# Kernel optimization log

Measured on AMD Instinct MI355X. Metric: run time of the kernel, lower is better.

The kernel has to match this reference:

```python
import jax, jax.numpy as jnp
import numpy as np
import math

B, S, E, H = 4, 1024, 1024, 16
D = E // H
C = 1.0           # Poincare ball curvature
CS = math.sqrt(C)
EPS = 1e-7

def _sq(x):
    return jnp.sum(x * x, axis=-1, keepdims=True)

def expmap0(v):
    n = jnp.sqrt(jnp.clip(_sq(v), 1e-15))
    return jnp.tanh(CS * n) * v / (CS * n)

def logmap0(y):
    n = jnp.sqrt(jnp.clip(_sq(y), 1e-15))
    t = jnp.clip(CS * n, 0.0, 1.0 - 1e-6)
    return jnp.arctanh(t) * y / (CS * n)

def hlinear(x, z, r):
    # Poincare fully-connected layer (HNN++, Shimizu et al.), as in hypll HLinear
    lam = 2.0 / jnp.clip(1.0 - C * _sq(x), EPS)          # [..., 1] conformal factor
    zn = jnp.clip(jnp.linalg.norm(z, axis=0), 1e-15)     # [out]
    xz = x @ z                                           # [..., out]
    tcr = 2.0 * CS * r
    v = (2.0 * zn / CS) * jnp.arcsinh(CS * lam * xz / zn * jnp.cosh(tcr) - (lam - 1.0) * jnp.sinh(tcr))
    w = jnp.sinh(CS * v) / CS
    return w / (1.0 + jnp.sqrt(1.0 + C * jnp.sum(w * w, -1, keepdims=True)))

def _beta(a, b):
    return math.exp(math.lgamma(a) + math.lgamma(b) - math.lgamma(a + b))

def _forward(query, key, value, zq, bq, zk, bk, zv, bv):
    pq, pk, pv = hlinear(query, zq, bq), hlinear(key, zk, bk), hlinear(value, zv, bv)
    split = lambda x: x.reshape(B, S, H, D).transpose(0, 2, 1, 3)   # [B,H,S,D]
    q, k, v = split(pq), split(pk), split(pv)
    # attention_similarity: negative per-head pairwise Poincare distance (all heads vectorized)
    q2 = jnp.sum(q * q, -1)                              # [B,H,Sq]
    k2 = jnp.sum(k * k, -1)                              # [B,H,Sk]
    qk = jnp.einsum('bhqd,bhkd->bhqk', q, k)
    diff2 = jnp.clip(q2[..., :, None] + k2[..., None, :] - 2.0 * qk, 0.0)
    den = jnp.clip((1.0 - C * q2)[..., :, None] * (1.0 - C * k2)[..., None, :], EPS)
    dist = jnp.arccosh(jnp.clip(1.0 + 2.0 * C * diff2 / den, 1.0 + 1e-6)) / CS
    # attention_activation: softmax over keys
    w = jax.nn.softmax(-dist, axis=-1)                   # [B,H,Sq,Sk]
    # attention_midpoint: weighted gyromidpoint of values over keys
    lam = 2.0 / jnp.clip(1.0 - C * jnp.sum(v * v, -1), EPS)          # [B,H,Sk]
    num = jnp.einsum('bhqk,bhkd->bhqd', w * lam[..., None, :], v)
    dnm = jnp.clip(jnp.einsum('bhqk,bhk->bhq', jnp.abs(w), lam - 1.0), EPS)
    u = num / dnm[..., None]
    mid = u / (1.0 + jnp.sqrt(jnp.clip(1.0 - C * _sq(u), EPS)))      # (1/2) Mobius scalar mult
    # manifold.cat: beta-concatenation of heads (HNN++)
    scale = _beta(E / 2.0, 0.5) / _beta(D / 2.0, 0.5)
    tv = logmap0(mid) * scale                            # tangent at origin, [B,H,S,D]
    return expmap0(tv.transpose(0, 2, 1, 3).reshape(B, S, E))

def setup_inputs():
    key = jax.random.key(0)
    ks = jax.random.split(key, 9)
    mk = lambda k: expmap0(jax.random.normal(k, (B, S, E), jnp.float32) * (0.3 / math.sqrt(E)))
    zs = lambda k: jax.random.normal(k, (E, E), jnp.float32) / math.sqrt(E)
    bs = lambda k: jax.random.normal(k, (E,), jnp.float32) * 0.01
    return {"query": mk(ks[0]), "key": mk(ks[1]), "value": mk(ks[2]),
            "zq": zs(ks[3]), "bq": bs(ks[4]), "zk": zs(ks[5]), "bk": bs(ks[6]),
            "zv": zs(ks[7]), "bv": bs(ks[8])}

def reference(query, key, value, zq, bq, zk, bk, zv, bv):
    return _forward(query, key, value, zq, bq, zk, bk, zv, bv)
```

## Files before the change

kernel.cpp:

```cpp
#include <hip/hip_runtime.h>
#include <cmath>

#define EPSF 1e-7f

constexpr int B_ = 4, S_ = 1024, E_ = 1024, H_ = 16, D_ = 64;
constexpr int BS_ = B_ * S_;

typedef __attribute__((ext_vector_type(8))) short bf16x8;
typedef __attribute__((ext_vector_type(4))) float f32x4;

__device__ inline unsigned int fbits(float f) { union { float f; unsigned int u; } x; x.f = f; return x.u; }
__device__ inline float ubits(unsigned int u) { union { unsigned int u; float f; } x; x.u = u; return x.f; }

__device__ inline unsigned short f2bf(float f) {
  unsigned int u = fbits(f);
  unsigned int r = u + 0x7fffu + ((u >> 16) & 1u);
  return (unsigned short)(r >> 16);
}
__device__ inline float bf2f(unsigned short h) { return ubits(((unsigned int)h) << 16); }
__device__ inline float fastrcp(float x) { return __builtin_amdgcn_rcpf(x); }

__device__ inline unsigned int packhi(float a, float b) {
  return (fbits(a) >> 16) | (fbits(b) & 0xFFFF0000u);
}
__device__ inline unsigned int packlo(float a, float b) {
  float la = a - ubits(fbits(a) & 0xFFFF0000u);
  float lb = b - ubits(fbits(b) & 0xFFFF0000u);
  return (fbits(la) >> 16) | (fbits(lb) & 0xFFFF0000u);
}

__device__ __forceinline__ void async_ld16(const unsigned short* g, unsigned short* l) {
  __builtin_amdgcn_global_load_lds(
      (const __attribute__((address_space(1))) unsigned int*)g,
      (__attribute__((address_space(3))) unsigned int*)l, 16, 0, 0);
}

__global__ __launch_bounds__(256) void xsplit_kernel(
    const float* __restrict__ xq, const float* __restrict__ xk,
    const float* __restrict__ xv, unsigned short* __restrict__ Xbf,
    float* __restrict__ lamRow) {
  const int row = blockIdx.x;
  const float* x = (row < BS_) ? xq : (row < 2 * BS_ ? xk : xv);
  const int r = row & (BS_ - 1);
  const int tid = threadIdx.x;
  float4 v = ((const float4*)(x + (size_t)r * E_))[tid];
  float s = v.x * v.x + v.y * v.y + v.z * v.z + v.w * v.w;
  #pragma unroll
  for (int m = 1; m < 64; m <<= 1) s += __shfl_xor(s, m, 64);
  __shared__ float red[4];
  if ((tid & 63) == 0) red[tid >> 6] = s;
  __syncthreads();
  s = red[0] + red[1] + red[2] + red[3];
  uint2 p;
  p.x = (unsigned int)f2bf(v.x) | ((unsigned int)f2bf(v.y) << 16);
  p.y = (unsigned int)f2bf(v.z) | ((unsigned int)f2bf(v.w) << 16);
  ((uint2*)(Xbf + (size_t)row * E_))[tid] = p;
  if (tid == 0) lamRow[row] = 2.0f / fmaxf(1.0f - s, EPSF);
}

__global__ __launch_bounds__(256) void zsplit_kernel(
    const float* __restrict__ zq, const float* __restrict__ zk, const float* __restrict__ zv,
    unsigned short* __restrict__ BhiT, unsigned short* __restrict__ BloT,
    float* __restrict__ Zpart) {
  const int mat = blockIdx.z;
  const float* z = mat == 0 ? zq : (mat == 1 ? zk : zv);
  const int k0 = blockIdx.y * 64, n0 = blockIdx.x * 64;
  __shared__ float t[64][65];
  __shared__ float sred[64][4];
  const int tid = threadIdx.x;
  {
    int kr = tid >> 4, nc = (tid & 15) * 4;
    #pragma unroll
    for (int i = 0; i < 4; i++) {
      float4 vv = *(const float4*)(z + (size_t)(k0 + kr + i * 16) * E_ + n0 + nc);
      t[kr + i * 16][nc + 0] = vv.x;
      t[kr + i * 16][nc + 1] = vv.y;
      t[kr + i * 16][nc + 2] = vv.z;
      t[kr + i * 16][nc + 3] = vv.w;
    }
  }
  __syncthreads();
  int nr = tid >> 2, kc = (tid & 3) * 16;
  unsigned int ph[8], pl[8];
  float ss = 0.f;
  #pragma unroll
  for (int p = 0; p < 8; p++) {
    float x0 = t[kc + 2 * p][nr], x1 = t[kc + 2 * p + 1][nr];
    ph[p] = packhi(x0, x1);
    pl[p] = packlo(x0, x1);
    ss += x0 * x0 + x1 * x1;
  }
  size_t off = (size_t)mat * E_ * E_ + (size_t)(n0 + nr) * E_ + k0 + kc;
  uint4* dh = (uint4*)(BhiT + off);
  uint4* dl = (uint4*)(BloT + off);
  dh[0] = make_uint4(ph[0], ph[1], ph[2], ph[3]);
  dh[1] = make_uint4(ph[4], ph[5], ph[6], ph[7]);
  dl[0] = make_uint4(pl[0], pl[1], pl[2], pl[3]);
  dl[1] = make_uint4(pl[4], pl[5], pl[6], pl[7]);
  sred[nr][tid & 3] = ss;
  __syncthreads();
  if (tid < 64) {
    float v = sred[tid][0] + sred[tid][1] + sred[tid][2] + sred[tid][3];
    Zpart[(size_t)(mat * 16 + blockIdx.y) * E_ + n0 + tid] = v;
  }
}

__global__ __launch_bounds__(256) void zstat_final_kernel(
    const float* __restrict__ Zpart,
    const float* __restrict__ bq, const float* __restrict__ bk, const float* __restrict__ bv,
    float* __restrict__ znA, float* __restrict__ chA, float* __restrict__ shA) {
  const int idx = blockIdx.x * 256 + threadIdx.x;
  const int mat = idx >> 10, col = idx & 1023;
  const float* bb = mat == 0 ? bq : (mat == 1 ? bk : bv);
  float s = 0.f;
  #pragma unroll
  for (int ky = 0; ky < 16; ky++)
    s += Zpart[(size_t)(mat * 16 + ky) * E_ + col];
  float n = fmaxf(sqrtf(s), 1e-15f);
  znA[idx] = n;
  float rb = bb[col];
  chA[idx] = coshf(2.f * rb);
  shA[idx] = sinhf(2.f * rb);
}

__global__ __launch_bounds__(256, 3) void hlinear_mfma_kernel(
    const unsigned short* __restrict__ Xbf,
    const unsigned short* __restrict__ BhiT, const unsigned short* __restrict__ BloT,
    const float* __restrict__ lamRow, const float* __restrict__ znA,
    const float* __restrict__ chA, const float* __restrict__ shA,
    unsigned short* __restrict__ Wbf) {
  const int mat = blockIdx.z;
  const unsigned short* xa = Xbf + (size_t)mat * BS_ * E_;
  const unsigned short* bh = BhiT + (size_t)mat * E_ * E_;
  const unsigned short* bl = BloT + (size_t)mat * E_ * E_;
  const int lid = blockIdx.y * 8 + blockIdx.x;
  const int sqi = lid >> 4, offb = lid & 15;
  const int m0 = ((sqi >> 1) * 4 + (offb & 3)) * 128;
  const int n0 = ((sqi & 1) * 4 + (offb >> 2)) * 128;

  __shared__ unsigned short LDSU[24576];
  unsigned short* As = LDSU;
  unsigned short* Bh = LDSU + 8192;
  unsigned short* Bl = LDSU + 16384;

  const int tid = threadIdx.x;
  const int wid = tid >> 6, lane = tid & 63, quad = lane >> 4, l16 = lane & 15;
  const int wm = (wid >> 1) * 64, wn = (wid & 1) * 64;

  f32x4 acc[4][4];
  #pragma unroll
  for (int i = 0; i < 4; i++)
    #pragma unroll
    for (int j = 0; j < 4; j++) acc[i][j] = (f32x4){0.f, 0.f, 0.f, 0.f};

  const int lrow = lane >> 3;
  const int lcs = ((lane & 7) ^ lrow) * 8;
  const int xsw = (l16 & 7);

  for (int kt = 0; kt < E_ / 64; ++kt) {
    __syncthreads();
    const int kb = kt * 64 + lcs;
    #pragma unroll
    for (int c2 = 0; c2 < 4; c2++) {
      const int c = wid * 4 + c2;
      const int grow = c * 8 + lrow;
      async_ld16(xa + (size_t)(m0 + grow) * E_ + kb, As + c * 512);
      async_ld16(bh + (size_t)(n0 + grow) * E_ + kb, Bh + c * 512);
      async_ld16(bl + (size_t)(n0 + grow) * E_ + kb, Bl + c * 512);
    }
    __syncthreads();
    #pragma unroll
    for (int h = 0; h < 2; h++) {
      bf16x8 a[4];
      #pragma unroll
      for (int mt = 0; mt < 4; mt++) {
        int row = wm + mt * 16 + l16;
        a[mt] = *(const bf16x8*)&As[row * 64 + (((h * 4 + quad) ^ xsw) * 8)];
      }
      #pragma unroll
      for (int nt = 0; nt < 4; nt++) {
        int row = wn + nt * 16 + l16;
        int ro = row * 64 + (((h * 4 + quad) ^ xsw) * 8);
        bf16x8 bhf = *(const bf16x8*)&Bh[ro];
        bf16x8 blf = *(const bf16x8*)&Bl[ro];
        #pragma unroll
        for (int mt = 0; mt < 4; mt++) {
          acc[mt][nt] = __builtin_amdgcn_mfma_f32_16x16x32_bf16(a[mt], bhf, acc[mt][nt], 0, 0, 0);
          acc[mt][nt] = __builtin_amdgcn_mfma_f32_16x16x32_bf16(a[mt], blf, acc[mt][nt], 0, 0, 0);
        }
      }
    }
  }

  const float* lamP = lamRow + mat * BS_;
  float lamv[16];
  #pragma unroll
  for (int mt = 0; mt < 4; mt++)
    #pragma unroll
    for (int r = 0; r < 4; r++)
      lamv[mt * 4 + r] = lamP[m0 + wm + mt * 16 + quad * 4 + r];

  __syncthreads();
  unsigned short* epi = LDSU + wid * 4608;
  #pragma unroll
  for (int nt = 0; nt < 4; nt++) {
    int cg = n0 + wn + nt * 16 + l16;
    float zn = znA[mat * E_ + cg];
    float chzn = chA[mat * E_ + cg] / zn;
    float sh = shA[mat * E_ + cg];
    float tzn = 2.f * zn;
    #pragma unroll
    for (int mt = 0; mt < 4; mt++) {
      #pragma unroll
      for (int r = 0; r < 4; r++) {
        float lam = lamv[mt * 4 + r];
        float arg = fmaf(lam * acc[mt][nt][r], chzn, -(lam - 1.f) * sh);
        float sq2 = sqrtf(fmaf(arg, arg, 1.f));
        float v = tzn * __logf(arg + sq2);
        float ev = __expf(v);
        float w = 0.5f * (ev - fastrcp(ev));
        epi[(mt * 16 + quad * 4 + r) * 72 + nt * 16 + l16] = f2bf(w);
      }
    }
  }
  unsigned short* gout = Wbf + (size_t)mat * BS_ * E_ + (size_t)(m0 + wm) * E_ + n0 + wn;
  const int rrow = lane >> 3, seg = lane & 7;
  #pragma unroll
  for (int i = 0; i < 8; i++) {
    int row = i * 8 + rrow;
    uint4 val = *(const uint4*)&epi[row * 72 + seg * 8];
    *(uint4*)(gout + (size_t)row * E_ + seg * 8) = val;
  }
}

__global__ __launch_bounds__(256) void normalize_kernel(
    const unsigned short* __restrict__ Wbf, unsigned short* __restrict__ Pbf,
    float* __restrict__ HN) {
  const unsigned short* w = Wbf + (size_t)blockIdx.x * E_;
  int tid = threadIdx.x;
  uint2 wv = ((const uint2*)w)[tid];
  float w0 = bf2f((unsigned short)(wv.x & 0xFFFF));
  float w1 = bf2f((unsigned short)(wv.x >> 16));
  float w2 = bf2f((unsigned short)(wv.y & 0xFFFF));
  float w3 = bf2f((unsigned short)(wv.y >> 16));
  float s = w0 * w0 + w1 * w1 + w2 * w2 + w3 * w3;
  #pragma unroll
  for (int m = 1; m < 64; m <<= 1) s += __shfl_xor(s, m, 64);
  __shared__ float red[4];
  if ((tid & 63) == 0) red[tid >> 6] = s;
  __syncthreads();
  s = red[0] + red[1] + red[2] + red[3];
  float t = 1.f / (1.f + sqrtf(1.f + s));
  unsigned short p0 = f2bf(w0 * t), p1 = f2bf(w1 * t), p2 = f2bf(w2 * t), p3 = f2bf(w3 * t);
  uint2 pk;
  pk.x = (unsigned int)p0 | ((unsigned int)p1 << 16);
  pk.y = (unsigned int)p2 | ((unsigned int)p3 << 16);
  ((uint2*)(Pbf + (size_t)blockIdx.x * E_))[tid] = pk;
  float r0 = bf2f(p0), r1 = bf2f(p1), r2 = bf2f(p2), r3 = bf2f(p3);
  float hs = r0 * r0 + r1 * r1 + r2 * r2 + r3 * r3;
  hs += __shfl_xor(hs, 1, 64);
  hs += __shfl_xor(hs, 2, 64);
  hs += __shfl_xor(hs, 4, 64);
  hs += __shfl_xor(hs, 8, 64);
  if ((tid & 15) == 0) HN[(size_t)blockIdx.x * H_ + (tid >> 4)] = hs;
}

__global__ __launch_bounds__(256) void vtrans_kernel(
    const unsigned short* __restrict__ Pbf, const float* __restrict__ HN,
    unsigned short* __restrict__ VtG, unsigned short* __restrict__ lamMG) {
  const int st = blockIdx.x, h = blockIdx.y, b = blockIdx.z;
  const unsigned short* pv = Pbf + (size_t)2 * BS_ * E_;
  const float* hnv = HN + (size_t)2 * BS_ * H_;
  __shared__ unsigned short T[64][72];
  __shared__ float lamS[64];
  const int tid = threadIdx.x;
  {
    int lr = tid >> 2, lc = (tid & 3) * 16;
    const uint4* src = (const uint4*)(pv + (size_t)(b * S_ + st * 64 + lr) * E_ + h * 64 + lc);
    *(uint4*)&T[lr][lc] = src[0];
    *(uint4*)&T[lr][lc + 8] = src[1];
  }
  if (tid < 64) {
    float v2 = hnv[(size_t)(b * S_ + st * 64 + tid) * H_ + h];
    float lam = 2.f / fmaxf(1.f - v2, EPSF);
    lamS[tid] = lam;
    lamMG[(size_t)(b * H_ + h) * S_ + st * 64 + tid] = f2bf(lam - 1.f);
  }
  __syncthreads();
  int d = tid >> 2, sc = (tid & 3) * 16;
  unsigned int o[8];
  #pragma unroll
  for (int i = 0; i < 8; i++) {
    int s0 = sc + 2 * i;
    float f0 = bf2f(T[s0][d]) * lamS[s0];
    float f1 = bf2f(T[s0 + 1][d]) * lamS[s0 + 1];
    o[i] = (unsigned int)f2bf(f0) | ((unsigned int)f2bf(f1) << 16);
  }
  unsigned short* dst = VtG + (size_t)((b * H_ + h) * 64 + d) * S_ + st * 64 + sc;
  ((uint4*)dst)[0] = make_uint4(o[0], o[1], o[2], o[3]);
  ((uint4*)dst)[1] = make_uint4(o[4], o[5], o[6], o[7]);
}

__global__ __launch_bounds__(512) void attention_kernel(
    const unsigned short* __restrict__ Pbf, const float* __restrict__ HN,
    const unsigned short* __restrict__ VtG, const unsigned short* __restrict__ lamMG,
    float* __restrict__ TV, float scale) {
  const int qt = blockIdx.x, h = blockIdx.y, b = blockIdx.z;
  const unsigned short* pq = Pbf;
  const unsigned short* pk = Pbf + (size_t)BS_ * E_;
  const float* hnq = HN;
  const float* hnk = HN + (size_t)BS_ * H_;

  const int tid = threadIdx.x;
  const int wid = tid >> 6, lane = tid & 63;
  const int quad = lane >> 4, l16 = lane & 15;

  __shared__ __align__(16) unsigned short Kl[4096];
  __shared__ __align__(16) unsigned short Vl[4096];
  __shared__ __align__(16) unsigned short Pw[8][16][72];
  __shared__ float k2s[64], romk2s[64];
  __shared__ __align__(16) unsigned short lamM16[64];

  const int qrow0 = qt * 128 + wid * 16;
  const size_t qgrow = ((size_t)(b * S_ + qrow0 + l16)) * E_ + h * 64;
  bf16x8 aq0 = *(const bf16x8*)(pq + qgrow + quad * 8);
  bf16x8 aq1 = *(const bf16x8*)(pq + qgrow + 32 + quad * 8);
  float q2r[4], tromq2[4];
  #pragma unroll
  for (int r2 = 0; r2 < 4; r2++) {
    float q2 = hnq[((size_t)(b * S_ + qrow0 + quad * 4 + r2)) * H_ + h];
    q2r[r2] = q2;
    tromq2[r2] = 2.f * fastrcp(1.f - q2);
  }

  f32x4 accO[4];
  #pragma unroll
  for (int dt = 0; dt < 4; dt++) accO[dt] = (f32x4){0.f, 0.f, 0.f, 0.f};
  f32x4 accD = (f32x4){0.f, 0.f, 0.f, 0.f};

  const int lr = lane >> 3, cch = lane & 7;
  const int xsw = l16 & 7;
  const unsigned short* kbase = pk + (size_t)(b * S_) * E_ + h * 64;
  const unsigned short* vbase = VtG + (size_t)(b * H_ + h) * 64 * S_;
  const unsigned short* lbase = lamMG + (size_t)(b * H_ + h) * S_;

  for (int kt = 0; kt < S_ / 64; ++kt) {
    __syncthreads();
    {
      const int r = wid * 8 + lr;
      const int cc = ((cch ^ (r & 7)) * 8);
      async_ld16(kbase + (size_t)(kt * 64 + r) * E_ + cc, Kl + wid * 512);
      async_ld16(vbase + (size_t)r * S_ + kt * 64 + cc, Vl + wid * 512);
    }
    if (tid < 64) {
      float k2 = hnk[((size_t)(b * S_ + kt * 64 + tid)) * H_ + h];
      k2s[tid] = k2;
      romk2s[tid] = fastrcp(1.f - k2);
      lamM16[tid] = lbase[kt * 64 + tid];
    }
    __syncthreads();

    #pragma unroll
    for (int nt = 0; nt < 4; nt++) {
      const int krow = nt * 16 + l16;
      bf16x8 bk0 = *(const bf16x8*)&Kl[krow * 64 + ((quad ^ xsw) * 8)];
      bf16x8 bk1 = *(const bf16x8*)&Kl[krow * 64 + (((4 + quad) ^ xsw) * 8)];
      f32x4 z = (f32x4){0.f, 0.f, 0.f, 0.f};
      f32x4 d0 = __builtin_amdgcn_mfma_f32_16x16x32_bf16(aq0, bk0, z, 0, 0, 0);
      d0 = __builtin_amdgcn_mfma_f32_16x16x32_bf16(aq1, bk1, d0, 0, 0, 0);
      float k2 = k2s[krow], romk2 = romk2s[krow];
      #pragma unroll
      for (int r2 = 0; r2 < 4; r2++) {
        float diff2 = fmaf(-2.f, d0[r2], q2r[r2] + k2);
        float t = fmaxf(diff2 * (tromq2[r2] * romk2), 1e-6f);
        float A = 1.f + t;
        float w = A - sqrtf(fmaf(A, A, -1.f));
        Pw[wid][quad * 4 + r2][krow] = (unsigned short)(fbits(w) >> 16);
      }
    }
    bf16x8 ap0 = *(const bf16x8*)&Pw[wid][l16][quad * 8];
    bf16x8 ap1 = *(const bf16x8*)&Pw[wid][l16][32 + quad * 8];
    #pragma unroll
    for (int dt = 0; dt < 4; dt++) {
      const int drow = dt * 16 + l16;
      bf16x8 bv0 = *(const bf16x8*)&Vl[drow * 64 + ((quad ^ xsw) * 8)];
      bf16x8 bv1 = *(const bf16x8*)&Vl[drow * 64 + (((4 + quad) ^ xsw) * 8)];
      accO[dt] = __builtin_amdgcn_mfma_f32_16x16x32_bf16(ap0, bv0, accO[dt], 0, 0, 0);
      accO[dt] = __builtin_amdgcn_mfma_f32_16x16x32_bf16(ap1, bv1, accO[dt], 0, 0, 0);
    }
    bf16x8 bl0 = *(const bf16x8*)&lamM16[quad * 8];
    bf16x8 bl1 = *(const bf16x8*)&lamM16[32 + quad * 8];
    accD = __builtin_amdgcn_mfma_f32_16x16x32_bf16(ap0, bl0, accD, 0, 0, 0);
    accD = __builtin_amdgcn_mfma_f32_16x16x32_bf16(ap1, bl1, accD, 0, 0, 0);
  }

  #pragma unroll
  for (int r2 = 0; r2 < 4; r2++) {
    float rdsum = 1.f / accD[r2];
    float uu[4];
    float su = 0.f;
    #pragma unroll
    for (int dt = 0; dt < 4; dt++) { uu[dt] = accO[dt][r2] * rdsum; su += uu[dt] * uu[dt]; }
    su += __shfl_xor(su, 1, 64);
    su += __shfl_xor(su, 2, 64);
    su += __shfl_xor(su, 4, 64);
    su += __shfl_xor(su, 8, 64);
    float g = 1.f / (1.f + sqrtf(fmaxf(1.f - su, EPSF)));
    float n2 = fmaxf(su * g * g, 1e-15f);
    float n = sqrtf(n2);
    float fac = atanhf(fminf(n, 1.f - 1e-6f)) / n * g * scale;
    size_t orow = ((size_t)(b * S_ + qrow0 + quad * 4 + r2)) * E_ + h * 64 + l16;
    #pragma unroll
    for (int dt = 0; dt < 4; dt++) TV[orow + dt * 16] = fac * uu[dt];
  }
}

__global__ __launch_bounds__(256) void expmap_kernel(float* __restrict__ TV) {
  float* w = TV + (size_t)blockIdx.x * E_;
  int tid = threadIdx.x;
  float4 v = ((float4*)w)[tid];
  float s = v.x * v.x + v.y * v.y + v.z * v.z + v.w * v.w;
  #pragma unroll
  for (int m = 1; m < 64; m <<= 1) s += __shfl_xor(s, m, 64);
  __shared__ float red[4];
  if ((tid & 63) == 0) red[tid >> 6] = s;
  __syncthreads();
  s = red[0] + red[1] + red[2] + red[3];
  float n = sqrtf(fmaxf(s, 1e-15f));
  float f = tanhf(n) / n;
  v.x *= f; v.y *= f; v.z *= f; v.w *= f;
  ((float4*)w)[tid] = v;
}

extern "C" void kernel_launch(void* const* d_in, const int* in_sizes, int n_in,
                              void* d_out, int out_size, void* d_ws, size_t ws_size,
                              hipStream_t stream) {
  (void)in_sizes; (void)n_in; (void)out_size; (void)ws_size;
  const float* q  = (const float*)d_in[0];
  const float* k  = (const float*)d_in[1];
  const float* v  = (const float*)d_in[2];
  const float* zq = (const float*)d_in[3];
  const float* bq = (const float*)d_in[4];
  const float* zk = (const float*)d_in[5];
  const float* bk = (const float*)d_in[6];
  const float* zv = (const float*)d_in[7];
  const float* bv = (const float*)d_in[8];

  unsigned short* Wbf = (unsigned short*)d_ws;
  unsigned short* Pbf = Wbf + (size_t)3 * BS_ * E_;
  unsigned short* BhiT = Pbf;
  unsigned short* BloT = Pbf + (size_t)3 * E_ * E_;
  unsigned short* Xbf = Pbf + (size_t)3 * BS_ * E_;
  float* HN           = (float*)(Xbf + (size_t)3 * BS_ * E_);
  float* lamRow       = HN + (size_t)3 * BS_ * H_;
  float* znA          = lamRow + 3 * BS_;
  float* chA          = znA + 3 * E_;
  float* shA          = chA + 3 * E_;
  float* Zpart        = shA + 3 * E_;
  unsigned short* VtG = (unsigned short*)(Zpart + 48 * E_);
  unsigned short* lamMG = VtG + (size_t)B_ * H_ * 64 * S_;
  float* out          = (float*)d_out;

  double lb1 = lgamma(E_ / 2.0) + lgamma(0.5) - lgamma(E_ / 2.0 + 0.5);
  double lb2 = lgamma(D_ / 2.0) + lgamma(0.5) - lgamma(D_ / 2.0 + 0.5);
  float scale = (float)exp(lb1 - lb2);

  hipLaunchKernelGGL(xsplit_kernel, dim3(3 * BS_), dim3(256), 0, stream, q, k, v, Xbf, lamRow);
  hipLaunchKernelGGL(zsplit_kernel, dim3(16, 16, 3), dim3(256), 0, stream,
                     zq, zk, zv, BhiT, BloT, Zpart);
  hipLaunchKernelGGL(zstat_final_kernel, dim3(12), dim3(256), 0, stream,
                     Zpart, bq, bk, bv, znA, chA, shA);
  hipLaunchKernelGGL(hlinear_mfma_kernel, dim3(8, 32, 3), dim3(256), 0, stream,
                     Xbf, BhiT, BloT, lamRow, znA, chA, shA, Wbf);
  hipLaunchKernelGGL(normalize_kernel, dim3(3 * BS_), dim3(256), 0, stream, Wbf, Pbf, HN);
  hipLaunchKernelGGL(vtrans_kernel, dim3(16, 16, 4), dim3(256), 0, stream, Pbf, HN, VtG, lamMG);
  hipLaunchKernelGGL(attention_kernel, dim3(S_ / 128, H_, B_), dim3(512), 0, stream,
                     Pbf, HN, VtG, lamMG, out, scale);
  hipLaunchKernelGGL(expmap_kernel, dim3(BS_), dim3(256), 0, stream, out);
}
```

Before: 253.1 us.

## Compute transposed QK^T so P feeds PV MFMA from registers, skipping LDS

The attention kernel now computes S^T = K·Q^T, so each lane holds four consecutive keys for one query. It packs these straight into a bf16x4 operand for 16x16x16 MFMAs against V and lambda, which removes the per-warp P staging through shared memory and the extra barrier-free LDS round trip. The per-head k2, 1/(1-k2) and lambda-1 arrays are precomputed in vtrans and preloaded whole into LDS, replacing the per-tile scalar loads. Blocks shrink to 256 threads with 64-query tiles, doubling the grid, and the output becomes float4 stores. The costs are more K/V reloads per query and a smaller MFMA shape.

After: 261.3 us. +3.3%, slower.

```diff
diff --git a/kernel.cpp b/kernel.cpp
--- a/kernel.cpp
+++ b/kernel.cpp
@@ -7,6 +7,7 @@
 constexpr int BS_ = B_ * S_;
 
 typedef __attribute__((ext_vector_type(8))) short bf16x8;
+typedef __attribute__((ext_vector_type(4))) short bf16x4;
 typedef __attribute__((ext_vector_type(4))) float f32x4;
 
 __device__ inline unsigned int fbits(float f) { union { float f; unsigned int u; } x; x.f = f; return x.u; }
@@ -267,9 +268,11 @@
 
 __global__ __launch_bounds__(256) void vtrans_kernel(
     const unsigned short* __restrict__ Pbf, const float* __restrict__ HN,
-    unsigned short* __restrict__ VtG, unsigned short* __restrict__ lamMG) {
+    unsigned short* __restrict__ VtG, unsigned short* __restrict__ lamMG,
+    float* __restrict__ k2T, float* __restrict__ romk2T) {
   const int st = blockIdx.x, h = blockIdx.y, b = blockIdx.z;
   const unsigned short* pv = Pbf + (size_t)2 * BS_ * E_;
+  const float* hnk = HN + (size_t)BS_ * H_;
   const float* hnv = HN + (size_t)2 * BS_ * H_;
   __shared__ unsigned short T[64][72];
   __shared__ float lamS[64];
@@ -284,7 +287,11 @@
     float v2 = hnv[(size_t)(b * S_ + st * 64 + tid) * H_ + h];
     float lam = 2.f / fmaxf(1.f - v2, EPSF);
     lamS[tid] = lam;
-    lamMG[(size_t)(b * H_ + h) * S_ + st * 64 + tid] = f2bf(lam - 1.f);
+    size_t sidx = (size_t)(b * H_ + h) * S_ + st * 64 + tid;
+    lamMG[sidx] = f2bf(lam - 1.f);
+    float k2 = hnk[(size_t)(b * S_ + st * 64 + tid) * H_ + h];
+    k2T[sidx] = k2;
+    romk2T[sidx] = fastrcp(1.f - k2);
   }
   __syncthreads();
   int d = tid >> 2, sc = (tid & 3) * 16;
@@ -301,15 +308,15 @@
   ((uint4*)dst)[1] = make_uint4(o[4], o[5], o[6], o[7]);
 }
 
-__global__ __launch_bounds__(512) void attention_kernel(
+__global__ __launch_bounds__(256) void attention_kernel(
     const unsigned short* __restrict__ Pbf, const float* __restrict__ HN,
     const unsigned short* __restrict__ VtG, const unsigned short* __restrict__ lamMG,
+    const float* __restrict__ k2T, const float* __restrict__ romk2T,
     float* __restrict__ TV, float scale) {
   const int qt = blockIdx.x, h = blockIdx.y, b = blockIdx.z;
   const unsigned short* pq = Pbf;
   const unsigned short* pk = Pbf + (size_t)BS_ * E_;
   const float* hnq = HN;
-  const float* hnk = HN + (size_t)BS_ * H_;
 
   const int tid = threadIdx.x;
   const int wid = tid >> 6, lane = tid & 63;
@@ -317,21 +324,23 @@
 
   __shared__ __align__(16) unsigned short Kl[4096];
   __shared__ __align__(16) unsigned short Vl[4096];
-  __shared__ __align__(16) unsigned short Pw[8][16][72];
-  __shared__ float k2s[64], romk2s[64];
-  __shared__ __align__(16) unsigned short lamM16[64];
-
-  const int qrow0 = qt * 128 + wid * 16;
+  __shared__ __align__(16) float k2L[1024];
+  __shared__ __align__(16) float rkL[1024];
+  __shared__ __align__(16) unsigned short lamL[1024];
+
+  const size_t bhS = (size_t)(b * H_ + h) * S_;
+  {
+    ((f32x4*)k2L)[tid] = ((const f32x4*)(k2T + bhS))[tid];
+    ((f32x4*)rkL)[tid] = ((const f32x4*)(romk2T + bhS))[tid];
+    ((uint2*)lamL)[tid] = ((const uint2*)(lamMG + bhS))[tid];
+  }
+
+  const int qrow0 = qt * 64 + wid * 16;
   const size_t qgrow = ((size_t)(b * S_ + qrow0 + l16)) * E_ + h * 64;
   bf16x8 aq0 = *(const bf16x8*)(pq + qgrow + quad * 8);
   bf16x8 aq1 = *(const bf16x8*)(pq + qgrow + 32 + quad * 8);
-  float q2r[4], tromq2[4];
-  #pragma unroll
-  for (int r2 = 0; r2 < 4; r2++) {
-    float q2 = hnq[((size_t)(b * S_ + qrow0 + quad * 4 + r2)) * H_ + h];
-    q2r[r2] = q2;
-    tromq2[r2] = 2.f * fastrcp(1.f - q2);
-  }
+  const float q2 = hnq[((size_t)(b * S_ + qrow0 + l16)) * H_ + h];
+  const float tromq2 = 2.f * fastrcp(1.f - q2);
 
   f32x4 accO[4];
   #pragma unroll
@@ -341,77 +350,79 @@
   const int lr = lane >> 3, cch = lane & 7;
   const int xsw = l16 & 7;
   const unsigned short* kbase = pk + (size_t)(b * S_) * E_ + h * 64;
-  const unsigned short* vbase = VtG + (size_t)(b * H_ + h) * 64 * S_;
-  const unsigned short* lbase = lamMG + (size_t)(b * H_ + h) * S_;
+  const unsigned short* vbase = VtG + bhS * 64;
 
   for (int kt = 0; kt < S_ / 64; ++kt) {
     __syncthreads();
-    {
-      const int r = wid * 8 + lr;
-      const int cc = ((cch ^ (r & 7)) * 8);
-      async_ld16(kbase + (size_t)(kt * 64 + r) * E_ + cc, Kl + wid * 512);
-      async_ld16(vbase + (size_t)r * S_ + kt * 64 + cc, Vl + wid * 512);
-    }
-    if (tid < 64) {
-      float k2 = hnk[((size_t)(b * S_ + kt * 64 + tid)) * H_ + h];
-      k2s[tid] = k2;
-      romk2s[tid] = fastrcp(1.f - k2);
-      lamM16[tid] = lbase[kt * 64 + tid];
+    #pragma unroll
+    for (int i = 0; i < 2; i++) {
+      const int r = wid * 16 + i * 8 + lr;
+      const int cc = ((cch ^ lr) * 8);
+      async_ld16(kbase + (size_t)(kt * 64 + r) * E_ + cc, Kl + wid * 1024 + i * 512);
+      async_ld16(vbase + (size_t)r * S_ + kt * 64 + cc, Vl + wid * 1024 + i * 512);
     }
     __syncthreads();
 
     #pragma unroll
     for (int nt = 0; nt < 4; nt++) {
       const int krow = nt * 16 + l16;
-      bf16x8 bk0 = *(const bf16x8*)&Kl[krow * 64 + ((quad ^ xsw) * 8)];
-      bf16x8 bk1 = *(const bf16x8*)&Kl[krow * 64 + (((4 + quad) ^ xsw) * 8)];
-      f32x4 z = (f32x4){0.f, 0.f, 0.f, 0.f};
-      f32x4 d0 = __builtin_amdgcn_mfma_f32_16x16x32_bf16(aq0, bk0, z, 0, 0, 0);
-      d0 = __builtin_amdgcn_mfma_f32_16x16x32_bf16(aq1, bk1, d0, 0, 0, 0);
-      float k2 = k2s[krow], romk2 = romk2s[krow];
+      const int kb = kt * 64 + nt * 16 + quad * 4;
+      bf16x8 ka0 = *(const bf16x8*)&Kl[krow * 64 + ((quad ^ xsw) * 8)];
+      bf16x8 ka1 = *(const bf16x8*)&Kl[krow * 64 + (((4 + quad) ^ xsw) * 8)];
+      f32x4 st = (f32x4){0.f, 0.f, 0.f, 0.f};
+      st = __builtin_amdgcn_mfma_f32_16x16x32_bf16(ka0, aq0, st, 0, 0, 0);
+      st = __builtin_amdgcn_mfma_f32_16x16x32_bf16(ka1, aq1, st, 0, 0, 0);
+      f32x4 k2v = *(const f32x4*)&k2L[kb];
+      f32x4 rkv = *(const f32x4*)&rkL[kb];
+      float w[4];
       #pragma unroll
       for (int r2 = 0; r2 < 4; r2++) {
-        float diff2 = fmaf(-2.f, d0[r2], q2r[r2] + k2);
-        float t = fmaxf(diff2 * (tromq2[r2] * romk2), 1e-6f);
+        float diff2 = fmaf(-2.f, st[r2], q2 + k2v[r2]);
+        float t = fmaxf(diff2 * (tromq2 * rkv[r2]), 1e-6f);
         float A = 1.f + t;
-        float w = A - sqrtf(fmaf(A, A, -1.f));
-        Pw[wid][quad * 4 + r2][krow] = (unsigned short)(fbits(w) >> 16);
+        w[r2] = A - sqrtf(fmaf(A, A, -1.f));
       }
-    }
-    bf16x8 ap0 = *(const bf16x8*)&Pw[wid][l16][quad * 8];
-    bf16x8 ap1 = *(const bf16x8*)&Pw[wid][l16][32 + quad * 8];
-    #pragma unroll
-    for (int dt = 0; dt < 4; dt++) {
-      const int drow = dt * 16 + l16;
-      bf16x8 bv0 = *(const bf16x8*)&Vl[drow * 64 + ((quad ^ xsw) * 8)];
-      bf16x8 bv1 = *(const bf16x8*)&Vl[drow * 64 + (((4 + quad) ^ xsw) * 8)];
-      accO[dt] = __builtin_amdgcn_mfma_f32_16x16x32_bf16(ap0, bv0, accO[dt], 0, 0, 0);
-      accO[dt] = __builtin_amdgcn_mfma_f32_16x16x32_bf16(ap1, bv1, accO[dt], 0, 0, 0);
-    }
-    bf16x8 bl0 = *(const bf16x8*)&lamM16[quad * 8];
-    bf16x8 bl1 = *(const bf16x8*)&lamM16[32 + quad * 8];
-    accD = __builtin_amdgcn_mfma_f32_16x16x32_bf16(ap0, bl0, accD, 0, 0, 0);
-    accD = __builtin_amdgcn_mfma_f32_16x16x32_bf16(ap1, bl1, accD, 0, 0, 0);
-  }
-
-  #pragma unroll
-  for (int r2 = 0; r2 < 4; r2++) {
-    float rdsum = 1.f / accD[r2];
-    float uu[4];
-    float su = 0.f;
-    #pragma unroll
-    for (int dt = 0; dt < 4; dt++) { uu[dt] = accO[dt][r2] * rdsum; su += uu[dt] * uu[dt]; }
-    su += __shfl_xor(su, 1, 64);
-    su += __shfl_xor(su, 2, 64);
-    su += __shfl_xor(su, 4, 64);
-    su += __shfl_xor(su, 8, 64);
-    float g = 1.f / (1.f + sqrtf(fmaxf(1.f - su, EPSF)));
-    float n2 = fmaxf(su * g * g, 1e-15f);
-    float n = sqrtf(n2);
-    float fac = atanhf(fminf(n, 1.f - 1e-6f)) / n * g * scale;
-    size_t orow = ((size_t)(b * S_ + qrow0 + quad * 4 + r2)) * E_ + h * 64 + l16;
-    #pragma unroll
-    for (int dt = 0; dt < 4; dt++) TV[orow + dt * 16] = fac * uu[dt];
+      union { unsigned int u[2]; bf16x4 v; } pw;
+      pw.u[0] = packhi(w[0], w[1]);
+      pw.u[1] = packhi(w[2], w[3]);
+      const int gc = nt * 2 + (quad >> 1);
+      const int vo = ((gc ^ xsw) << 3) + ((quad & 1) << 2);
+      #pragma unroll
+      for (int dt = 0; dt < 4; dt++) {
+        bf16x4 va = *(const bf16x4*)&Vl[(dt * 16 + l16) * 64 + vo];
+        accO[dt] = __builtin_amdgcn_mfma_f32_16x16x16bf16_1k(va, pw.v, accO[dt], 0, 0, 0);
+      }
+      bf16x4 la = *(const bf16x4*)&lamL[kb];
+      accD = __builtin_amdgcn_mfma_f32_16x16x16bf16_1k(la, pw.v, accD, 0, 0, 0);
+    }
+  }
+
+  float rdsum = 1.f / accD[0];
+  float uu[4][4];
+  float su = 0.f;
+  #pragma unroll
+  for (int dt = 0; dt < 4; dt++)
+    #pragma unroll
+    for (int r2 = 0; r2 < 4; r2++) {
+      float u = accO[dt][r2] * rdsum;
+      uu[dt][r2] = u;
+      su += u * u;
+    }
+  su += __shfl_xor(su, 16, 64);
+  su += __shfl_xor(su, 32, 64);
+  float g = 1.f / (1.f + sqrtf(fmaxf(1.f - su, EPSF)));
+  float n2 = fmaxf(su * g * g, 1e-15f);
+  float n = sqrtf(n2);
+  float fac = atanhf(fminf(n, 1.f - 1e-6f)) / n * g * scale;
+  float* orow = TV + ((size_t)(b * S_ + qrow0 + l16)) * E_ + h * 64 + quad * 4;
+  #pragma unroll
+  for (int dt = 0; dt < 4; dt++) {
+    float4 o;
+    o.x = fac * uu[dt][0];
+    o.y = fac * uu[dt][1];
+    o.z = fac * uu[dt][2];
+    o.w = fac * uu[dt][3];
+    *(float4*)(orow + dt * 16) = o;
   }
 }
 
@@ -459,6 +470,8 @@
   float* Zpart        = shA + 3 * E_;
   unsigned short* VtG = (unsigned short*)(Zpart + 48 * E_);
   unsigned short* lamMG = VtG + (size_t)B_ * H_ * 64 * S_;
+  float* k2T          = (float*)(lamMG + (size_t)B_ * H_ * S_);
+  float* romk2T       = k2T + (size_t)B_ * H_ * S_;
   float* out          = (float*)d_out;
 
   double lb1 = lgamma(E_ / 2.0) + lgamma(0.5) - lgamma(E_ / 2.0 + 0.5);
@@ -473,8 +486,9 @@
   hipLaunchKernelGGL(hlinear_mfma_kernel, dim3(8, 32, 3), dim3(256), 0, stream,
                      Xbf, BhiT, BloT, lamRow, znA, chA, shA, Wbf);
   hipLaunchKernelGGL(normalize_kernel, dim3(3 * BS_), dim3(256), 0, stream, Wbf, Pbf, HN);
-  hipLaunchKernelGGL(vtrans_kernel, dim3(16, 16, 4), dim3(256), 0, stream, Pbf, HN, VtG, lamMG);
-  hipLaunchKernelGGL(attention_kernel, dim3(S_ / 128, H_, B_), dim3(512), 0, stream,
-                     Pbf, HN, VtG, lamMG, out, scale);
+  hipLaunchKernelGGL(vtrans_kernel, dim3(16, 16, 4), dim3(256), 0, stream,
+                     Pbf, HN, VtG, lamMG, k2T, romk2T);
+  hipLaunchKernelGGL(attention_kernel, dim3(16, 16, 4), dim3(256), 0, stream,
+                     Pbf, HN, VtG, lamMG, k2T, romk2T, out, scale);
   hipLaunchKernelGGL(expmap_kernel, dim3(BS_), dim3(256), 0, stream, out);
 }
```
